# Optimization experiments

Measured on AMD Instinct MI355X. Metric: run time of the kernel, lower is better.

The kernel has to match this reference:

```python
import jax, jax.numpy as jnp
import numpy as np

B, S, D = 1, 1024, 4096
NH, NKV, HD = 32, 8, 128
CACHE = 1024


def setup_inputs() -> dict:
    key = jax.random.key(0)
    ks = jax.random.split(key, 9)
    return {
        "hidden_states": jax.random.normal(ks[0], (B, S, D), jnp.float32),
        "freqs_cos": jax.random.uniform(ks[1], (S, HD // 2), jnp.float32),
        "freqs_sin": jax.random.uniform(ks[2], (S, HD // 2), jnp.float32),
        "atten_mask": jnp.zeros((S, CACHE + S), jnp.float32),
        "k_cache": jax.random.normal(ks[3], (B, NKV, HD, CACHE), jnp.float32),
        "v_cache": jax.random.normal(ks[4], (B, NKV, CACHE, HD), jnp.float32),
        "wq": jax.random.normal(ks[5], (NH, HD, D), jnp.float32) * 0.02,
        "wk": jax.random.normal(ks[6], (NKV, HD, D), jnp.float32) * 0.02,
        "wv": jax.random.normal(ks[7], (NKV, HD, D), jnp.float32) * 0.02,
        "wo": jax.random.normal(ks[8], (D, NH * HD), jnp.float32) * 0.02,
    }


def _rope(x, cos, sin):
    # x: [b, s, h, hd]; cos/sin: [s, hd//2]
    half = x.shape[-1] // 2
    xr, xi = x[..., :half], x[..., half:]
    c = cos[None, :, None, :]
    sn = sin[None, :, None, :]
    return jnp.concatenate([xr * c - xi * sn, xr * sn + xi * c], axis=-1)


def reference(hidden_states, freqs_cos, freqs_sin, atten_mask, k_cache, v_cache, wq, wk, wv, wo):
    b, s, d = hidden_states.shape
    nh, hd, _ = wq.shape
    nkv = wk.shape[0]
    g = nh // nkv  # query heads per KV head
    scale = float(hd) ** 0.5

    # projections (equivalent to per-head 1x1 convs)
    q = jnp.einsum("bsd,hed->bshe", hidden_states, wq)   # [b,s,nh,hd]
    k = jnp.einsum("bsd,hed->bshe", hidden_states, wk)   # [b,s,nkv,hd]
    v = jnp.einsum("bsd,hed->bshe", hidden_states, wv)   # [b,s,nkv,hd]

    q = _rope(q, freqs_cos, freqs_sin)
    k = _rope(k, freqs_cos, freqs_sin)

    # concat KV cache: kh [b,nkv,hd,KV], vh [b,nkv,KV,hd]
    kh = jnp.concatenate([k_cache, k.transpose(0, 2, 3, 1)], axis=-1)
    vh = jnp.concatenate([v_cache, v.transpose(0, 2, 1, 3)], axis=2)

    # grouped attention: head i uses kv group i // g
    qg = q.reshape(b, s, nkv, g, hd).transpose(0, 2, 3, 1, 4)  # [b,n,g,s,e]
    scores = jnp.einsum("bngse,bnet->bngst", qg, kh) / scale + atten_mask
    p = jax.nn.softmax(scores, axis=-1)
    yg = jnp.einsum("bngst,bnte->bngse", p, vh)               # [b,n,g,s,e]
    y = yg.transpose(0, 3, 1, 2, 4).reshape(b, s, nh * hd)     # head order n*g+j

    y = jnp.einsum("bsf,df->bsd", y, wo)
    return (y, kh, vh)
```

## Files before the change

kernel.cpp:

```cpp
#include <hip/hip_runtime.h>
#include <hip/hip_bf16.h>
#include <stdint.h>

#define S_LEN 1024
#define D_MODEL 4096
#define NHEAD 32
#define NKV 8
#define HD 128
#define CACHE_T 1024
#define T_TOT 2048
#define NQKV 6144
#define QSCALE 0.08838834764831845f

typedef __attribute__((ext_vector_type(8))) short short8;
typedef __attribute__((ext_vector_type(4))) float floatx4;
typedef __attribute__((ext_vector_type(16))) float floatx16;

__device__ __forceinline__ unsigned short f2bf(float f) {
  union { float f; uint32_t u; } v; v.f = f;
  uint32_t r = v.u + 0x7FFFu + ((v.u >> 16) & 1u);
  return (unsigned short)(r >> 16);
}

__device__ __forceinline__ unsigned pack2bf(float a, float b) {
  union { __hip_bfloat162 h2; unsigned u; } c;
  c.h2 = __float22bfloat162_rn(make_float2(a, b));
  return c.u;
}

__device__ __forceinline__ void gload_lds16(const void* g, void* s) {
  __builtin_amdgcn_global_load_lds((const __attribute__((address_space(1))) void*)g,
                                   (__attribute__((address_space(3))) void*)s, 16, 0, 0);
}

__device__ __forceinline__ void conv8(const float* __restrict__ in, unsigned short* __restrict__ out, int idx) {
  int i = idx * 8;
  floatx4 a = *(const floatx4*)(in + i);
  floatx4 b = *(const floatx4*)(in + i + 4);
  short8 o;
  o[0] = (short)f2bf(a[0]); o[1] = (short)f2bf(a[1]); o[2] = (short)f2bf(a[2]); o[3] = (short)f2bf(a[3]);
  o[4] = (short)f2bf(b[0]); o[5] = (short)f2bf(b[1]); o[6] = (short)f2bf(b[2]); o[7] = (short)f2bf(b[3]);
  *(short8*)(out + i) = o;
}

__global__ void convf2b_kernel(const float* __restrict__ in, unsigned short* __restrict__ out, int n8) {
  int stride = gridDim.x * blockDim.x;
  for (int t = blockIdx.x * blockDim.x + threadIdx.x; t < n8; t += stride)
    conv8(in, out, t);
}

__global__ void mask_flag_kernel(const float* __restrict__ m, int n, int* __restrict__ flag) {
  int stride = gridDim.x * blockDim.x;
  bool nz = false;
  for (int i = blockIdx.x * blockDim.x + threadIdx.x; i < n; i += stride)
    nz |= (m[i] != 0.0f);
  if (nz) atomicOr(flag, 1);
}

__global__ void front_kernel(const float* __restrict__ mask, int nmask, int* __restrict__ flag,
                             const float* __restrict__ hs, unsigned short* __restrict__ hs_b,
                             const float* __restrict__ wq, const float* __restrict__ wk,
                             const float* __restrict__ wv, unsigned short* __restrict__ slotW)
{
  const int b = blockIdx.x, tid = threadIdx.x;
  if (b < 256) {
    bool nz = false;
    for (int i = b * 256 + tid; i < nmask; i += 256 * 256)
      nz |= (mask[i] != 0.0f);
    if (nz) atomicOr(flag, 1);
  } else if (b < 2304) {
    conv8(hs, hs_b, (b - 256) * 256 + tid);
  } else if (b < 10496) {
    conv8(wq, slotW, (b - 2304) * 256 + tid);
  } else if (b < 12544) {
    conv8(wk, slotW + (size_t)4096 * 4096, (b - 10496) * 256 + tid);
  } else {
    conv8(wv, slotW + (size_t)5120 * 4096, (b - 12544) * 256 + tid);
  }
}

__global__ __launch_bounds__(256, 3)
void gemm_bf_kernel(const unsigned short* __restrict__ A,
                    const unsigned short* __restrict__ W,
                    float* __restrict__ C,
                    int M, int N, int K, int ldc, int GM)
{
  __shared__ __align__(16) unsigned char As[2][64 * 128];
  __shared__ __align__(16) unsigned char Bs[2][128 * 128];

  const int nwg = gridDim.x;
  int orig = blockIdx.x;
  int wg = (orig & 7) * (nwg >> 3) + (orig >> 3);
  const int mt = wg % GM, nt = wg / GM;
  const int m0 = mt * 64, n0 = nt * 128;

  const int tid = threadIdx.x;
  const int wid = tid >> 6, lane = tid & 63;
  const int g4 = lane >> 4, r16 = lane & 15;
  const int wr = (wid >> 1) * 32, wc = (wid & 1) * 64;

  const int lr = lane >> 3, lc = lane & 7;
  const unsigned short* Arow[2];
  const unsigned short* Wrow[4];
#pragma unroll
  for (int i = 0; i < 2; ++i) {
    int r = (wid * 2 + i) * 8 + lr;
    Arow[i] = A + (size_t)(m0 + r) * K + (lc ^ (r & 7)) * 8;
  }
#pragma unroll
  for (int i = 0; i < 4; ++i) {
    int r = (wid * 4 + i) * 8 + lr;
    Wrow[i] = W + (size_t)(n0 + r) * K + (lc ^ (r & 7)) * 8;
  }

  auto stage = [&](int buf, int kt) {
    const int kb = kt * 64;
#pragma unroll
    for (int i = 0; i < 2; ++i)
      gload_lds16(Arow[i] + kb, &As[buf][(wid * 2 + i) * 1024]);
#pragma unroll
    for (int i = 0; i < 4; ++i)
      gload_lds16(Wrow[i] + kb, &Bs[buf][(wid * 4 + i) * 1024]);
  };

  floatx4 acc[2][4];
#pragma unroll
  for (int m = 0; m < 2; ++m)
#pragma unroll
    for (int n = 0; n < 4; ++n) acc[m][n] = (floatx4){0.f, 0.f, 0.f, 0.f};

  const int NK = K >> 6;
  stage(0, 0);
  __syncthreads();
  int cur = 0;
  for (int kt = 0; kt < NK; ++kt) {
    if (kt + 1 < NK) stage(cur ^ 1, kt + 1);
#pragma unroll
    for (int kk = 0; kk < 2; ++kk) {
      const int kb = kk * 64 + g4 * 16;
      short8 af[2], bf[4];
#pragma unroll
      for (int m = 0; m < 2; ++m) {
        int row = wr + m * 16 + r16;
        af[m] = *(const short8*)(&As[cur][row * 128 + (kb ^ ((row & 7) << 4))]);
      }
#pragma unroll
      for (int n = 0; n < 4; ++n) {
        int row = wc + n * 16 + r16;
        bf[n] = *(const short8*)(&Bs[cur][row * 128 + (kb ^ ((row & 7) << 4))]);
      }
#pragma unroll
      for (int m = 0; m < 2; ++m)
#pragma unroll
        for (int n = 0; n < 4; ++n)
          acc[m][n] = __builtin_amdgcn_mfma_f32_16x16x32_bf16(af[m], bf[n], acc[m][n], 0, 0, 0);
    }
    __syncthreads();
    cur ^= 1;
  }

#pragma unroll
  for (int m = 0; m < 2; ++m)
#pragma unroll
    for (int n = 0; n < 4; ++n)
#pragma unroll
      for (int j = 0; j < 4; ++j)
        C[(size_t)(m0 + wr + m * 16 + g4 * 4 + j) * ldc + (n0 + wc + n * 16 + r16)] = acc[m][n][j];
}

__global__ __launch_bounds__(256, 2)
void gemm_kernel(const unsigned short* __restrict__ A,
                 const float* __restrict__ W0, const float* __restrict__ W1, const float* __restrict__ W2,
                 int n1, int n2,
                 float* __restrict__ C,
                 int M, int N, int K, int GM)
{
  __shared__ __align__(16) unsigned char As[2][128 * 128];
  __shared__ __align__(16) unsigned char Bs[2][128 * 128];

  const int nwg = gridDim.x;
  int orig = blockIdx.x;
  int xcd = orig & 7, loc = orig >> 3;
  int q = nwg >> 3, r = nwg & 7;
  int wg = (xcd < r ? xcd * (q + 1) : r * (q + 1) + (xcd - r) * q) + loc;
  const int mt = wg % GM, nt = wg / GM;
  const int m0 = mt * 128, n0 = nt * 128;

  const int tid = threadIdx.x;
  const int wid = tid >> 6, lane = tid & 63;
  const int g4 = lane >> 4, r16 = lane & 15;
  const int wr = (wid >> 1) * 64, wc = (wid & 1) * 64;

  int srow[4], skc[4];
  const float* wptr[4];
#pragma unroll
  for (int i = 0; i < 4; ++i) {
    int c = tid + 256 * i;
    srow[i] = c >> 3; skc[i] = c & 7;
    int ng = n0 + srow[i];
    wptr[i] = (ng < n1) ? (W0 + (size_t)ng * K)
            : (ng < n2) ? (W1 + (size_t)(ng - n1) * K)
                        : (W2 + (size_t)(ng - n2) * K);
  }

  short8 ar[4]; floatx4 br[8];
  auto load_tile = [&](int kt) {
    int kb = kt * 64;
#pragma unroll
    for (int i = 0; i < 4; ++i) {
      ar[i] = *(const short8*)(A + (size_t)(m0 + srow[i]) * K + kb + skc[i] * 8);
      br[2 * i]     = *(const floatx4*)(wptr[i] + kb + skc[i] * 8);
      br[2 * i + 1] = *(const floatx4*)(wptr[i] + kb + skc[i] * 8 + 4);
    }
  };
  auto write_tile = [&](int buf) {
#pragma unroll
    for (int i = 0; i < 4; ++i) {
      int off = srow[i] * 128 + ((skc[i] * 16) ^ ((srow[i] & 7) << 4));
      *(short8*)(&As[buf][off]) = ar[i];
      short8 bb;
      bb[0] = (short)f2bf(br[2 * i][0]);     bb[1] = (short)f2bf(br[2 * i][1]);
      bb[2] = (short)f2bf(br[2 * i][2]);     bb[3] = (short)f2bf(br[2 * i][3]);
      bb[4] = (short)f2bf(br[2 * i + 1][0]); bb[5] = (short)f2bf(br[2 * i + 1][1]);
      bb[6] = (short)f2bf(br[2 * i + 1][2]); bb[7] = (short)f2bf(br[2 * i + 1][3]);
      *(short8*)(&Bs[buf][off]) = bb;
    }
  };

  floatx4 acc[4][4];
#pragma unroll
  for (int m = 0; m < 4; ++m)
#pragma unroll
    for (int n = 0; n < 4; ++n) acc[m][n] = (floatx4){0.f, 0.f, 0.f, 0.f};

  const int NK = K >> 6;
  load_tile(0);
  write_tile(0);
  __syncthreads();
  int cur = 0;
  for (int kt = 0; kt < NK; ++kt) {
    if (kt + 1 < NK) load_tile(kt + 1);
#pragma unroll
    for (int kk = 0; kk < 2; ++kk) {
      const int kb = kk * 32 + g4 * 8;
      short8 af[4], bfr[4];
#pragma unroll
      for (int m = 0; m < 4; ++m) {
        int row = wr + m * 16 + r16;
        af[m] = *(const short8*)(&As[cur][row * 128 + ((kb * 2) ^ ((row & 7) << 4))]);
      }
#pragma unroll
      for (int n = 0; n < 4; ++n) {
        int row = wc + n * 16 + r16;
        bfr[n] = *(const short8*)(&Bs[cur][row * 128 + ((kb * 2) ^ ((row & 7) << 4))]);
      }
#pragma unroll
      for (int m = 0; m < 4; ++m)
#pragma unroll
        for (int n = 0; n < 4; ++n)
          acc[m][n] = __builtin_amdgcn_mfma_f32_16x16x32_bf16(af[m], bfr[n], acc[m][n], 0, 0, 0);
    }
    if (kt + 1 < NK) write_tile(cur ^ 1);
    __syncthreads();
    cur ^= 1;
  }

#pragma unroll
  for (int m = 0; m < 4; ++m)
#pragma unroll
    for (int n = 0; n < 4; ++n)
#pragma unroll
      for (int j = 0; j < 4; ++j)
        C[(size_t)(m0 + wr + m * 16 + g4 * 4 + j) * N + (n0 + wc + n * 16 + r16)] = acc[m][n][j];
}

__global__ void prep_all_kernel(const float* __restrict__ qkv, const float* __restrict__ fc,
                                const float* __restrict__ fs, const float* __restrict__ kc,
                                const float* __restrict__ vc,
                                unsigned short* __restrict__ qb,
                                float* __restrict__ kh, unsigned short* __restrict__ khb,
                                float* __restrict__ vh, unsigned short* __restrict__ vtb)
{
  __shared__ __align__(16) unsigned char smem[128 * 65 * 4];
  const int blk = blockIdx.x, tid = threadIdx.x;

  if (blk < 1024) {
    const int s = blk;
    const int head = tid >> 3, e0 = (tid & 7) * 8;
    const float* base = qkv + (size_t)s * NQKV + head * HD + e0;
    floatx4 xr0 = *(const floatx4*)(base);
    floatx4 xr1 = *(const floatx4*)(base + 4);
    floatx4 xi0 = *(const floatx4*)(base + 64);
    floatx4 xi1 = *(const floatx4*)(base + 68);
    floatx4 c0 = *(const floatx4*)(fc + s * 64 + e0);
    floatx4 c1 = *(const floatx4*)(fc + s * 64 + e0 + 4);
    floatx4 s0 = *(const floatx4*)(fs + s * 64 + e0);
    floatx4 s1 = *(const floatx4*)(fs + s * 64 + e0 + 4);
    short8 outr, outi;
#pragma unroll
    for (int j = 0; j < 4; ++j) {
      outr[j]     = (short)f2bf((xr0[j] * c0[j] - xi0[j] * s0[j]) * QSCALE);
      outr[4 + j] = (short)f2bf((xr1[j] * c1[j] - xi1[j] * s1[j]) * QSCALE);
      outi[j]     = (short)f2bf((xr0[j] * s0[j] + xi0[j] * c0[j]) * QSCALE);
      outi[4 + j] = (short)f2bf((xr1[j] * s1[j] + xi1[j] * c1[j]) * QSCALE);
    }
    unsigned short* ob = qb + (size_t)s * D_MODEL + head * HD + e0;
    *(short8*)ob = outr;
    *(short8*)(ob + 64) = outi;
  } else if (blk < 1408) {
    const int bb = blk - 1024;
    if (bb < 128) {
      float (*T)[65] = (float(*)[65])smem;
      const int n = bb >> 4, s0 = (bb & 15) * 64;
      const int sl = tid >> 2, e0 = (tid & 3) * 16;
      const int s = s0 + sl;
      const float* base = qkv + (size_t)s * NQKV + D_MODEL + n * HD;
      float xr[16], xi[16], cc[16], sn[16];
#pragma unroll
      for (int i = 0; i < 16; i += 4) {
        *(floatx4*)(xr + i) = *(const floatx4*)(base + e0 + i);
        *(floatx4*)(xi + i) = *(const floatx4*)(base + 64 + e0 + i);
        *(floatx4*)(cc + i) = *(const floatx4*)(fc + s * 64 + e0 + i);
        *(floatx4*)(sn + i) = *(const floatx4*)(fs + s * 64 + e0 + i);
      }
      short8 r0, r1, i0, i1;
#pragma unroll
      for (int i = 0; i < 16; ++i) {
        float vr = xr[i] * cc[i] - xi[i] * sn[i];
        float vi = xr[i] * sn[i] + xi[i] * cc[i];
        T[e0 + i][sl] = vr;
        T[64 + e0 + i][sl] = vi;
        unsigned short br = f2bf(vr), bi = f2bf(vi);
        if (i < 8) { r0[i] = (short)br; i0[i] = (short)bi; }
        else       { r1[i - 8] = (short)br; i1[i - 8] = (short)bi; }
      }
      unsigned short* kb = khb + ((size_t)n * T_TOT + CACHE_T + s) * HD;
      *(short8*)(kb + e0) = r0;       *(short8*)(kb + e0 + 8) = r1;
      *(short8*)(kb + 64 + e0) = i0;  *(short8*)(kb + 64 + e0 + 8) = i1;
      __syncthreads();
      const int e = tid >> 1, hf = tid & 1;
      float* dst = kh + ((size_t)n * HD + e) * T_TOT + CACHE_T + s0 + hf * 32;
#pragma unroll
      for (int i = 0; i < 32; i += 4) {
        floatx4 v;
        v[0] = T[e][hf * 32 + i]; v[1] = T[e][hf * 32 + i + 1];
        v[2] = T[e][hf * 32 + i + 2]; v[3] = T[e][hf * 32 + i + 3];
        *(floatx4*)(dst + i) = v;
      }
    } else {
      unsigned short (*T)[72] = (unsigned short(*)[72])smem;
      const int b = bb - 128;
      const int n = b >> 5, et = (b >> 4) & 1, tt = b & 15;
      const int e0 = et * 64, t0 = tt * 64;
      const int el = tid >> 2, tc = (tid & 3) * 16;
      const float* src = kc + ((size_t)n * HD + e0 + el) * CACHE_T + t0 + tc;
      float* dst = kh + ((size_t)n * HD + e0 + el) * T_TOT + t0 + tc;
#pragma unroll
      for (int i = 0; i < 16; i += 4) {
        floatx4 v = *(const floatx4*)(src + i);
        *(floatx4*)(dst + i) = v;
        T[tc + i][el] = f2bf(v[0]); T[tc + i + 1][el] = f2bf(v[1]);
        T[tc + i + 2][el] = f2bf(v[2]); T[tc + i + 3][el] = f2bf(v[3]);
      }
      __syncthreads();
      const int tl = tid >> 2, ec = (tid & 3) * 16;
      unsigned short* ob = khb + ((size_t)n * T_TOT + t0 + tl) * HD + e0 + ec;
#pragma unroll
      for (int i = 0; i < 16; i += 8) *(short8*)(ob + i) = *(const short8*)(&T[tl][ec + i]);
    }
  } else {
    const int bb = blk - 1408;
    unsigned short (*T)[72] = (unsigned short(*)[72])smem;
    if (bb < 128) {
      const int n = bb >> 4, s0 = (bb & 15) * 64;
      const int sl = tid >> 2, e0 = (tid & 3) * 32;
      const float* src = qkv + (size_t)(s0 + sl) * NQKV + D_MODEL + NKV * HD + n * HD + e0;
      float* dst = vh + ((size_t)n * T_TOT + CACHE_T + s0 + sl) * HD + e0;
#pragma unroll
      for (int i = 0; i < 32; i += 4) {
        floatx4 v = *(const floatx4*)(src + i);
        *(floatx4*)(dst + i) = v;
        T[e0 + i][sl] = f2bf(v[0]); T[e0 + i + 1][sl] = f2bf(v[1]);
        T[e0 + i + 2][sl] = f2bf(v[2]); T[e0 + i + 3][sl] = f2bf(v[3]);
      }
      __syncthreads();
      const int e = tid >> 1, hf = tid & 1;
      unsigned short* ob = vtb + ((size_t)n * HD + e) * T_TOT + CACHE_T + s0 + hf * 32;
#pragma unroll
      for (int i = 0; i < 32; i += 8) *(short8*)(ob + i) = *(const short8*)(&T[e][hf * 32 + i]);
    } else {
      const int b = bb - 128;
      const int n = b >> 4, t0 = (b & 15) * 64;
      const int tl = tid >> 2, e0 = (tid & 3) * 32;
      const float* src = vc + ((size_t)n * CACHE_T + t0 + tl) * HD + e0;
      float* dst = vh + ((size_t)n * T_TOT + t0 + tl) * HD + e0;
#pragma unroll
      for (int i = 0; i < 32; i += 4) {
        floatx4 v = *(const floatx4*)(src + i);
        *(floatx4*)(dst + i) = v;
        T[e0 + i][tl] = f2bf(v[0]); T[e0 + i + 1][tl] = f2bf(v[1]);
        T[e0 + i + 2][tl] = f2bf(v[2]); T[e0 + i + 3][tl] = f2bf(v[3]);
      }
      __syncthreads();
      const int e = tid >> 1, hf = tid & 1;
      unsigned short* ob = vtb + ((size_t)n * HD + e) * T_TOT + t0 + hf * 32;
#pragma unroll
      for (int i = 0; i < 32; i += 8) *(short8*)(ob + i) = *(const short8*)(&T[e][hf * 32 + i]);
    }
  }
}

__global__ __launch_bounds__(256, 2)
void attn_kernel(const unsigned short* __restrict__ Qb, const unsigned short* __restrict__ Kb,
                 const unsigned short* __restrict__ Vb, const float* __restrict__ mask,
                 const int* __restrict__ flag, unsigned short* __restrict__ Ob,
                 float* __restrict__ Upart, float* __restrict__ mlpart, int nsplit)
{
  __shared__ __align__(16) unsigned char KL[2][64 * 256];
  __shared__ __align__(16) unsigned char VL[2][128 * 128];

  const int nwg = gridDim.x;
  int orig = blockIdx.x;
  int wg = (orig & 7) * (nwg >> 3) + (orig >> 3);
  const int per_n = 32 * nsplit;
  const int nkv = wg / per_n;
  const int rem = wg % per_n;
  const int kvs = rem >> 5;
  const int inner = rem & 31;
  const int h = nkv * 4 + (inner >> 3);
  const int qt = inner & 7;
  const int TKV = T_TOT / nsplit;

  const int tid = threadIdx.x, wid = tid >> 6, lane = tid & 63;
  const int l31 = lane & 31, hi = lane >> 5;
  const int qrow = qt * 128 + wid * 32 + l31;
  const bool use_mask = (*flag) != 0;

  short8 qf[8];
#pragma unroll
  for (int c = 0; c < 8; ++c)
    qf[c] = *(const short8*)(Qb + (size_t)qrow * D_MODEL + h * HD + c * 16 + hi * 8);

  floatx16 acc[4];
#pragma unroll
  for (int et = 0; et < 4; ++et)
    acc[et] = (floatx16){0.f,0.f,0.f,0.f,0.f,0.f,0.f,0.f,0.f,0.f,0.f,0.f,0.f,0.f,0.f,0.f};
  float m = -1e30f, l = 0.f;

  const unsigned short* Kbase = Kb + (size_t)nkv * T_TOT * HD + (size_t)kvs * TKV * HD;
  const unsigned short* Vbase = Vb + (size_t)nkv * HD * T_TOT + (size_t)kvs * TKV;

  const unsigned short* kp[4];
  const unsigned short* vp[4];
  int kbase_off[4], vbase_off[4];
#pragma unroll
  for (int i = 0; i < 4; ++i) {
    int krow = wid * 16 + i * 4 + (lane >> 4);
    int kch  = (lane & 15) ^ (krow & 7);
    kp[i] = Kbase + (size_t)krow * HD + kch * 8;
    kbase_off[i] = (wid * 16 + i * 4) * 256;
    int vrow = wid * 32 + i * 8 + (lane >> 3);
    int vch  = (lane & 7) ^ (vrow & 7);
    vp[i] = Vbase + (size_t)vrow * T_TOT + vch * 8;
    vbase_off[i] = (wid * 32 + i * 8) * 128;
  }

#pragma unroll
  for (int i = 0; i < 4; ++i) gload_lds16(kp[i], &KL[0][kbase_off[i]]);
#pragma unroll
  for (int i = 0; i < 4; ++i) gload_lds16(vp[i], &VL[0][vbase_off[i]]);
#pragma unroll
  for (int i = 0; i < 4; ++i) { kp[i] += 64 * HD; vp[i] += 64; }
  __syncthreads();

  int cur = 0;
  for (int t0 = 0; t0 < TKV; t0 += 64) {
    if (t0 + 64 < TKV) {
#pragma unroll
      for (int i = 0; i < 4; ++i) gload_lds16(kp[i], &KL[cur ^ 1][kbase_off[i]]);
#pragma unroll
      for (int i = 0; i < 4; ++i) gload_lds16(vp[i], &VL[cur ^ 1][vbase_off[i]]);
#pragma unroll
      for (int i = 0; i < 4; ++i) { kp[i] += 64 * HD; vp[i] += 64; }
    }

    floatx16 sc[2];
#pragma unroll
    for (int ts = 0; ts < 2; ++ts) {
      sc[ts] = (floatx16){0.f,0.f,0.f,0.f,0.f,0.f,0.f,0.f,0.f,0.f,0.f,0.f,0.f,0.f,0.f,0.f};
      const int krow = ts * 32 + l31;
      const int swz = (krow & 7) << 4;
      const unsigned char* kr = &KL[cur][krow * 256];
#pragma unroll
      for (int c = 0; c < 8; ++c) {
        short8 kf = *(const short8*)(kr + ((c * 32 + hi * 16) ^ swz));
        sc[ts] = __builtin_amdgcn_mfma_f32_32x32x16_bf16(kf, qf[c], sc[ts], 0, 0, 0);
      }
    }

    if (use_mask) {
#pragma unroll
      for (int ts = 0; ts < 2; ++ts)
#pragma unroll
        for (int r = 0; r < 16; ++r) {
          int tg = kvs * TKV + t0 + ts * 32 + (r & 3) + 8 * (r >> 2) + 4 * hi;
          sc[ts][r] += mask[(size_t)qrow * T_TOT + tg];
        }
    }

    float pm = sc[0][0];
#pragma unroll
    for (int r = 1; r < 16; ++r) pm = fmaxf(pm, sc[0][r]);
#pragma unroll
    for (int r = 0; r < 16; ++r) pm = fmaxf(pm, sc[1][r]);
    pm = fmaxf(pm, __shfl_xor(pm, 32));

    if (__any(pm > m + 8.f)) {
      float nm = fmaxf(m, pm);
      float corr = __expf(m - nm);
      m = nm; l *= corr;
#pragma unroll
      for (int r = 0; r < 16; ++r) {
        float cr = __shfl(corr, (r & 3) + 8 * (r >> 2) + 4 * hi);
#pragma unroll
        for (int et = 0; et < 4; ++et) acc[et][r] *= cr;
      }
    }

    unsigned cpk[4][4];
    float ls = 0.f;
#pragma unroll
    for (int ts = 0; ts < 2; ++ts)
#pragma unroll
      for (int i = 0; i < 8; ++i) {
        float plo = __expf(sc[ts][2 * i] - m);
        float phi = __expf(sc[ts][2 * i + 1] - m);
        ls += plo + phi;
        cpk[ts * 2 + (i >> 2)][i & 3] = pack2bf(plo, phi);
      }
    ls += __shfl_xor(ls, 32);
    l += ls;

    short8 pa[4];
#pragma unroll
    for (int tc = 0; tc < 4; ++tc) {
      unsigned s0 = (unsigned)__shfl_xor((int)cpk[tc][0], 32);
      unsigned s1 = (unsigned)__shfl_xor((int)cpk[tc][1], 32);
      unsigned s2 = (unsigned)__shfl_xor((int)cpk[tc][2], 32);
      unsigned s3 = (unsigned)__shfl_xor((int)cpk[tc][3], 32);
      union { unsigned u[4]; short8 v; } fr;
      fr.u[0] = hi ? s2 : cpk[tc][0];
      fr.u[1] = hi ? s3 : cpk[tc][1];
      fr.u[2] = hi ? cpk[tc][2] : s0;
      fr.u[3] = hi ? cpk[tc][3] : s1;
      pa[tc] = fr.v;
    }

#pragma unroll
    for (int et = 0; et < 4; ++et) {
      const int vrow = et * 32 + l31;
      const int swz = (vrow & 7) << 4;
      const unsigned char* vr = &VL[cur][vrow * 128];
#pragma unroll
      for (int tc = 0; tc < 4; ++tc) {
        short8 vf = *(const short8*)(vr + ((tc * 32 + hi * 16) ^ swz));
        acc[et] = __builtin_amdgcn_mfma_f32_32x32x16_bf16(pa[tc], vf, acc[et], 0, 0, 0);
      }
    }
    __syncthreads();
    cur ^= 1;
  }

  if (nsplit == 2) {
    float* Ub = Upart + (size_t)kvs * (NHEAD * S_LEN) * HD;
#pragma unroll
    for (int et = 0; et < 4; ++et)
#pragma unroll
      for (int r = 0; r < 16; ++r) {
        int q = qt * 128 + wid * 32 + (r & 3) + 8 * (r >> 2) + 4 * hi;
        Ub[((size_t)h * S_LEN + q) * HD + et * 32 + l31] = acc[et][r];
      }
    if (lane < 32) {
      float* mlp = mlpart + ((size_t)kvs * (NHEAD * S_LEN) + (size_t)h * S_LEN + qrow) * 2;
      mlp[0] = m; mlp[1] = l;
    }
  } else {
    float inv = 1.0f / l;
#pragma unroll
    for (int et = 0; et < 4; ++et)
#pragma unroll
      for (int r = 0; r < 16; ++r) {
        float ir = __shfl(inv, (r & 3) + 8 * (r >> 2) + 4 * hi);
        int q = qt * 128 + wid * 32 + (r & 3) + 8 * (r >> 2) + 4 * hi;
        Ob[(size_t)q * D_MODEL + h * HD + et * 32 + l31] = f2bf(acc[et][r] * ir);
      }
  }
}

__global__ void attn_combine_kernel(const float* __restrict__ U, const float* __restrict__ ml,
                                    unsigned short* __restrict__ Ob)
{
  const int t = blockIdx.x * 256 + threadIdx.x;
  const int r = t >> 4;
  const int e0 = (t & 15) * 8;
  const float m1 = ml[(size_t)r * 2],                     l1 = ml[(size_t)r * 2 + 1];
  const float m2 = ml[((size_t)(NHEAD * S_LEN) + r) * 2], l2 = ml[((size_t)(NHEAD * S_LEN) + r) * 2 + 1];
  const float M = fmaxf(m1, m2);
  const float a1 = __expf(m1 - M), a2 = __expf(m2 - M);
  const float inv = 1.0f / (l1 * a1 + l2 * a2);
  const float* u1 = U + (size_t)r * HD + e0;
  const float* u2 = U + (size_t)(NHEAD * S_LEN) * HD + (size_t)r * HD + e0;
  floatx4 x1a = *(const floatx4*)u1, x1b = *(const floatx4*)(u1 + 4);
  floatx4 x2a = *(const floatx4*)u2, x2b = *(const floatx4*)(u2 + 4);
  const int s = r & (S_LEN - 1), hh = r >> 10;
  unsigned short* ob = Ob + (size_t)s * D_MODEL + hh * HD + e0;
  short8 o;
#pragma unroll
  for (int k = 0; k < 4; ++k) {
    o[k]     = (short)f2bf((x1a[k] * a1 + x2a[k] * a2) * inv);
    o[4 + k] = (short)f2bf((x1b[k] * a1 + x2b[k] * a2) * inv);
  }
  *(short8*)ob = o;
}

extern "C" void kernel_launch(void* const* d_in, const int* in_sizes, int n_in,
                              void* d_out, int out_size, void* d_ws, size_t ws_size,
                              hipStream_t stream)
{
  const float* hs   = (const float*)d_in[0];
  const float* fc   = (const float*)d_in[1];
  const float* fs   = (const float*)d_in[2];
  const float* mask = (const float*)d_in[3];
  const float* kc   = (const float*)d_in[4];
  const float* vc   = (const float*)d_in[5];
  const float* wq   = (const float*)d_in[6];
  const float* wk   = (const float*)d_in[7];
  const float* wv   = (const float*)d_in[8];
  const float* wo   = (const float*)d_in[9];

  float* y  = (float*)d_out;
  float* kh = y + (size_t)S_LEN * D_MODEL;
  float* vh = kh + (size_t)NKV * HD * T_TOT;

  char* ws = (char*)d_ws;
  unsigned short* hs_b   = (unsigned short*)ws;
  float* qkv             = (float*)(ws + 8388608u);
  unsigned short* attn_o = (unsigned short*)(ws + 8388608u);
  unsigned short* khb    = (unsigned short*)(ws + 33554432u);
  unsigned short* vtb    = (unsigned short*)(ws + 37748736u);
  int* flag              = (int*)(ws + 41943040u);
  unsigned short* slotW  = (unsigned short*)(ws + 41943296u);

  const size_t base = 41943296ull;
  const bool big = ws_size >= base + 50331648ull;
  const bool mid = ws_size >= base + 33554432ull;
  const int nsplit = (ws_size >= base + 34078720ull) ? 2 : 1;
  float* Upart  = (float*)(ws + base);
  float* mlpart = (float*)(ws + base + 33554432u);

  hipMemsetAsync(flag, 0, 4, stream);

  if (big) {
    front_kernel<<<14592, 256, 0, stream>>>(mask, S_LEN * T_TOT, flag, hs, hs_b,
                                            wq, wk, wv, slotW);
    gemm_bf_kernel<<<768, 256, 0, stream>>>(hs_b, slotW, qkv, 1024, 6144, 4096, 6144, 16);
  } else if (mid) {
    mask_flag_kernel<<<256, 256, 0, stream>>>(mask, S_LEN * T_TOT, flag);
    convf2b_kernel<<<2048, 256, 0, stream>>>(hs, hs_b, S_LEN * D_MODEL / 8);
    convf2b_kernel<<<2048, 256, 0, stream>>>(wk, slotW, NKV * HD * D_MODEL / 8);
    convf2b_kernel<<<2048, 256, 0, stream>>>(wv, slotW + (size_t)1024 * 4096, NKV * HD * D_MODEL / 8);
    gemm_bf_kernel<<<256, 256, 0, stream>>>(hs_b, slotW, qkv + 4096, 1024, 2048, 4096, 6144, 16);
    convf2b_kernel<<<2048, 256, 0, stream>>>(wq, slotW, NHEAD * HD * D_MODEL / 8);
    gemm_bf_kernel<<<512, 256, 0, stream>>>(hs_b, slotW, qkv, 1024, 4096, 4096, 6144, 16);
  } else {
    mask_flag_kernel<<<256, 256, 0, stream>>>(mask, S_LEN * T_TOT, flag);
    convf2b_kernel<<<2048, 256, 0, stream>>>(hs, hs_b, S_LEN * D_MODEL / 8);
    gemm_kernel<<<384, 256, 0, stream>>>(hs_b, wq, wk, wv, 4096, 5120, qkv, 1024, 6144, 4096, 8);
  }

  prep_all_kernel<<<1664, 256, 0, stream>>>(qkv, fc, fs, kc, vc, hs_b, kh, khb, vh, vtb);

  attn_kernel<<<256 * nsplit, 256, 0, stream>>>(hs_b, khb, vtb, mask, flag, attn_o,
                                                Upart, mlpart, nsplit);
  if (nsplit == 2)
    attn_combine_kernel<<<2048, 256, 0, stream>>>(Upart, mlpart, attn_o);

  if (mid) {
    convf2b_kernel<<<2048, 256, 0, stream>>>(wo, slotW, D_MODEL * D_MODEL / 8);
    gemm_bf_kernel<<<512, 256, 0, stream>>>(attn_o, slotW, y, 1024, 4096, 4096, 4096, 16);
  } else {
    gemm_kernel<<<256, 256, 0, stream>>>(attn_o, wo, wo, wo, 1 << 29, 1 << 29, y, 1024, 4096, 4096, 8);
  }
}
```

Before: 241.6 us.

## Split-K output projection GEMM with 64x128 tiles and a separate reduction kernel

On the large-workspace path, the output-projection GEMM becomes a split-K kernel. It uses 64x128 tiles and two K halves, launching 1024 workgroups with a target of three per CU instead of 512 larger tiles. Each half writes an fp32 partial into workspace, and a separate add kernel sums the two partials into y. The goal is more parallelism and better CU balance for this GEMM. The cost is an extra 32 MB fp32 write-and-read round trip, one more kernel launch, and less data reuse per tile.

```diff
diff --git a/kernel.cpp b/kernel.cpp
--- a/kernel.cpp
+++ b/kernel.cpp
@@ -168,6 +168,111 @@
         C[(size_t)(m0 + wr + m * 16 + g4 * 4 + j) * ldc + (n0 + wc + n * 16 + r16)] = acc[m][n][j];
 }
 
+__global__ __launch_bounds__(256, 3)
+void gemm_bf_ks_kernel(const unsigned short* __restrict__ A,
+                       const unsigned short* __restrict__ W,
+                       float* __restrict__ P0, float* __restrict__ P1)
+{
+  __shared__ __align__(16) unsigned char As[2][64 * 128];
+  __shared__ __align__(16) unsigned char Bs[2][128 * 128];
+
+  const int K = 4096, ldc = 4096, GM = 16, NK = 32;
+  const int nwg = gridDim.x;
+  int orig = blockIdx.x;
+  int wg = (orig & 7) * (nwg >> 3) + (orig >> 3);
+  const int ks = wg >> 9;
+  const int inner = wg & 511;
+  const int mt = inner % GM, nt = inner / GM;
+  const int m0 = mt * 64, n0 = nt * 128;
+  const int kofs = ks * 2048;
+
+  const int tid = threadIdx.x;
+  const int wid = tid >> 6, lane = tid & 63;
+  const int g4 = lane >> 4, r16 = lane & 15;
+  const int wr = (wid >> 1) * 32, wc = (wid & 1) * 64;
+
+  const int lr = lane >> 3, lc = lane & 7;
+  const unsigned short* Arow[2];
+  const unsigned short* Wrow[4];
+#pragma unroll
+  for (int i = 0; i < 2; ++i) {
+    int r = (wid * 2 + i) * 8 + lr;
+    Arow[i] = A + (size_t)(m0 + r) * K + kofs + (lc ^ (r & 7)) * 8;
+  }
+#pragma unroll
+  for (int i = 0; i < 4; ++i) {
+    int r = (wid * 4 + i) * 8 + lr;
+    Wrow[i] = W + (size_t)(n0 + r) * K + kofs + (lc ^ (r & 7)) * 8;
+  }
+
+  auto stage = [&](int buf, int kt) {
+    const int kb = kt * 64;
+#pragma unroll
+    for (int i = 0; i < 2; ++i)
+      gload_lds16(Arow[i] + kb, &As[buf][(wid * 2 + i) * 1024]);
+#pragma unroll
+    for (int i = 0; i < 4; ++i)
+      gload_lds16(Wrow[i] + kb, &Bs[buf][(wid * 4 + i) * 1024]);
+  };
+
+  floatx4 acc[2][4];
+#pragma unroll
+  for (int m = 0; m < 2; ++m)
+#pragma unroll
+    for (int n = 0; n < 4; ++n) acc[m][n] = (floatx4){0.f, 0.f, 0.f, 0.f};
+
+  stage(0, 0);
+  __syncthreads();
+  int cur = 0;
+  for (int kt = 0; kt < NK; ++kt) {
+    if (kt + 1 < NK) stage(cur ^ 1, kt + 1);
+#pragma unroll
+    for (int kk = 0; kk < 2; ++kk) {
+      const int kb = kk * 64 + g4 * 16;
+      short8 af[2], bf[4];
+#pragma unroll
+      for (int m = 0; m < 2; ++m) {
+        int row = wr + m * 16 + r16;
+        af[m] = *(const short8*)(&As[cur][row * 128 + (kb ^ ((row & 7) << 4))]);
+      }
+#pragma unroll
+      for (int n = 0; n < 4; ++n) {
+        int row = wc + n * 16 + r16;
+        bf[n] = *(const short8*)(&Bs[cur][row * 128 + (kb ^ ((row & 7) << 4))]);
+      }
+#pragma unroll
+      for (int m = 0; m < 2; ++m)
+#pragma unroll
+        for (int n = 0; n < 4; ++n)
+          acc[m][n] = __builtin_amdgcn_mfma_f32_16x16x32_bf16(af[m], bf[n], acc[m][n], 0, 0, 0);
+    }
+    __syncthreads();
+    cur ^= 1;
+  }
+
+  float* Cd = ks ? P1 : P0;
+#pragma unroll
+  for (int m = 0; m < 2; ++m)
+#pragma unroll
+    for (int n = 0; n < 4; ++n)
+#pragma unroll
+      for (int j = 0; j < 4; ++j)
+        Cd[(size_t)(m0 + wr + m * 16 + g4 * 4 + j) * ldc + (n0 + wc + n * 16 + r16)] = acc[m][n][j];
+}
+
+__global__ void add2_kernel(const float* __restrict__ p0, const float* __restrict__ p1,
+                            float* __restrict__ y)
+{
+  const int i = (blockIdx.x * 256 + threadIdx.x) * 8;
+  floatx4 a0 = *(const floatx4*)(p0 + i),     a1 = *(const floatx4*)(p0 + i + 4);
+  floatx4 b0 = *(const floatx4*)(p1 + i),     b1 = *(const floatx4*)(p1 + i + 4);
+  floatx4 r0, r1;
+#pragma unroll
+  for (int k = 0; k < 4; ++k) { r0[k] = a0[k] + b0[k]; r1[k] = a1[k] + b1[k]; }
+  *(floatx4*)(y + i) = r0;
+  *(floatx4*)(y + i + 4) = r1;
+}
+
 __global__ __launch_bounds__(256, 2)
 void gemm_kernel(const unsigned short* __restrict__ A,
                  const float* __restrict__ W0, const float* __restrict__ W1, const float* __restrict__ W2,
@@ -646,6 +751,7 @@
   unsigned short* hs_b   = (unsigned short*)ws;
   float* qkv             = (float*)(ws + 8388608u);
   unsigned short* attn_o = (unsigned short*)(ws + 8388608u);
+  float* p0              = (float*)(ws + 16777216u);
   unsigned short* khb    = (unsigned short*)(ws + 33554432u);
   unsigned short* vtb    = (unsigned short*)(ws + 37748736u);
   int* flag              = (int*)(ws + 41943040u);
@@ -657,6 +763,7 @@
   const int nsplit = (ws_size >= base + 34078720ull) ? 2 : 1;
   float* Upart  = (float*)(ws + base);
   float* mlpart = (float*)(ws + base + 33554432u);
+  float* p1     = (float*)(ws + base + 33554432u);
 
   hipMemsetAsync(flag, 0, 4, stream);
 
@@ -685,7 +792,11 @@
   if (nsplit == 2)
     attn_combine_kernel<<<2048, 256, 0, stream>>>(Upart, mlpart, attn_o);
 
-  if (mid) {
+  if (big) {
+    convf2b_kernel<<<2048, 256, 0, stream>>>(wo, slotW, D_MODEL * D_MODEL / 8);
+    gemm_bf_ks_kernel<<<1024, 256, 0, stream>>>(attn_o, slotW, p0, p1);
+    add2_kernel<<<2048, 256, 0, stream>>>(p0, p1, y);
+  } else if (mid) {
     convf2b_kernel<<<2048, 256, 0, stream>>>(wo, slotW, D_MODEL * D_MODEL / 8);
     gemm_bf_kernel<<<512, 256, 0, stream>>>(attn_o, slotW, y, 1024, 4096, 4096, 4096, 16);
   } else {
```

Result: slower. 253.6 us (+5.0%).
